# Kernel tuning notes

Hardware: AMD Instinct MI355X
Metric: run time of the kernel (lower is better)

The kernel has to match this reference:

```python
import jax, jax.numpy as jnp
import numpy as np

EPS = 1e-6
SEARCH_RANGE = 4  # K = 2*R+1 = 9


def setup_inputs() -> dict:
    key = jax.random.key(0)
    k1, k2, k3, k4 = jax.random.split(key, 4)
    B, C, H, W = 4, 128, 128, 240
    E = 64
    F_L = jax.random.normal(k1, (B, C, H, W), dtype=jnp.float32)
    F_R = jax.random.normal(k2, (B, C, H, W), dtype=jnp.float32)
    d0 = jax.random.uniform(k3, (B, 1, H, W), dtype=jnp.float32) * 64.0  # pixel disparity
    phi_w = jax.random.normal(k4, (E, C), dtype=jnp.float32) / np.sqrt(C)  # 1x1 conv weight
    return {"F_L": F_L, "F_R": F_R, "d0": d0, "phi_w": phi_w}


def _embed(x, phi_w):
    # 1x1 conv + channel L2 normalize (cosine embedding)
    y = jnp.einsum('ec,bchw->behw', phi_w, x)
    norm = jnp.sqrt(jnp.sum(y * y, axis=1, keepdims=True)) + EPS
    return y / norm


def reference(F_L, F_R, d0, phi_w):
    R = SEARCH_RANGE
    FL = _embed(F_L, phi_w)  # (B,E,H,W)
    FR = _embed(F_R, phi_w)
    B, E, H, W = FL.shape
    deltas = jnp.arange(-R, R + 1, dtype=FL.dtype)  # (K,)
    xx = jnp.arange(W, dtype=FL.dtype)  # base x grid
    # x' = x - (d0 + delta); align_corners=True grid round-trips to pixel coords exactly,
    # y coordinate is identity, so warp is 1D bilinear along W with border clamp.
    xprime = xx[None, None, None, :] - d0[:, None, 0, :, :] - deltas[None, :, None, None]  # (B,K,H,W)
    x0 = jnp.floor(xprime)
    w = xprime - x0  # bilinear weight
    i0 = jnp.clip(x0.astype(jnp.int32), 0, W - 1)
    i1 = jnp.clip(x0.astype(jnp.int32) + 1, 0, W - 1)
    FR_e = FR[:, None]  # (B,1,E,H,W)
    g0 = jnp.take_along_axis(FR_e, i0[:, :, None, :, :], axis=4)  # (B,K,E,H,W)
    g1 = jnp.take_along_axis(FR_e, i1[:, :, None, :, :], axis=4)
    FR_s = g0 * (1.0 - w)[:, :, None] + g1 * w[:, :, None]
    cost_vol = jnp.einsum('behw,bkehw->bkhw', FL, FR_s)  # (B,K,H,W)
    return cost_vol
```

## Files before the change

### kernel.cpp

```cpp
#include <hip/hip_runtime.h>
#include <hip/hip_bf16.h>

#define NB 4
#define NC 128
#define NH 128
#define NW 240
#define NE 64
#define NK 9
#define PLANE (NH*NW)
#define CHW (NC*PLANE)

typedef __attribute__((ext_vector_type(8))) short short8;
typedef __attribute__((ext_vector_type(4))) float f32x4;
typedef __attribute__((ext_vector_type(2))) __fp16 fp16x2;
typedef __attribute__((ext_vector_type(8))) __fp16 fp16x8;

__device__ __forceinline__ unsigned pkh(float x, float y){
  fp16x2 h = __builtin_amdgcn_cvt_pkrtz(x, y);
  return __builtin_bit_cast(unsigned, h);
}
__device__ __forceinline__ float fdot2u(unsigned a, unsigned b, float c){
#if __has_builtin(__builtin_amdgcn_fdot2)
  return __builtin_amdgcn_fdot2(__builtin_bit_cast(fp16x2,a),
                                __builtin_bit_cast(fp16x2,b), c, false);
#else
  fp16x2 ha = __builtin_bit_cast(fp16x2,a), hb = __builtin_bit_cast(fp16x2,b);
  return c + (float)ha[0]*(float)hb[0] + (float)ha[1]*(float)hb[1];
#endif
}
__device__ __forceinline__ int swz(int r){ return (r ^ (r>>3)) & 7; }

__device__ __forceinline__ void gload_lds16(const float* g, float* lds_u, int lane){
#if __has_builtin(__builtin_amdgcn_global_load_lds)
  __builtin_amdgcn_global_load_lds(
      (const __attribute__((address_space(1))) unsigned*)g,
      (__attribute__((address_space(3))) unsigned*)lds_u, 16, 0, 0);
#else
  *(float4*)(lds_u + 4*lane) = *(const float4*)g;
#endif
}

#define WAITB(N) do {                                                        \
    asm volatile("s_waitcnt vmcnt(" #N ") lgkmcnt(0)" ::: "memory");         \
    __builtin_amdgcn_s_barrier();                                            \
    __builtin_amdgcn_sched_barrier(0);                                       \
  } while (0)

__global__ __launch_bounds__(1024, 4)
void fused_kernel(const float* __restrict__ xL,
                  const float* __restrict__ xR,
                  const float* __restrict__ d0g,
                  const float* __restrict__ phig,
                  float* __restrict__ outg)
{
  __shared__ __attribute__((aligned(16))) float bufs[4*7680];
  __shared__ __attribute__((aligned(16))) unsigned short phis[NE*136];

  const int tid  = threadIdx.x;
  const int lane = tid & 63;
  const int wv   = tid >> 6;
  const int b    = blockIdx.x >> 7;
  const int h    = blockIdx.x & 127;
  const size_t base = (size_t)b*CHW + (size_t)h*NW;
  const int pixbase = (b*NH + h)*NW;

  const int mrow = lane & 15;
  const int kg   = lane >> 4;
  const int nt   = wv;
  const int n    = 16*nt + mrow;

  auto issue_chunk = [&](int q){
    const float* src = (q < 4) ? xL : xR;
    const int cb = 32*(q & 3);
    float* buf = &bufs[(q & 3)*7680];
    #pragma unroll
    for (int i = 0; i < 2; ++i) {
      int qq = 2*wv + i;
      if (qq < 30) {
        int g4 = qq*64 + lane;
        int c = g4/60, s4 = g4 - 60*c;
        gload_lds16(src + base + (size_t)(cb + c)*PLANE + 4*s4,
                    buf + qq*256, lane);
      }
    }
  };

  auto gemm_round = [&](const float* bf, int cb, f32x4 (&acc)[4]){
    if (nt < 15) {
      fp16x8 bv;
      #pragma unroll
      for (int j = 0; j < 8; ++j)
        bv[j] = (__fp16)bf[(8*kg + j)*240 + n];
      #pragma unroll
      for (int mt = 0; mt < 4; ++mt) {
        short8 raw = *(const short8*)&phis[(16*mt + mrow)*136 + cb + 8*kg];
        fp16x8 af = __builtin_bit_cast(fp16x8, raw);
        acc[mt] = __builtin_amdgcn_mfma_f32_16x16x32_f16(af, bv, acc[mt], 0, 0, 0);
      }
    }
  };

  auto norm_pack = [&](f32x4 (&acc)[4], uint2 (&pk)[4]){
    float ss = 0.f;
    #pragma unroll
    for (int mt = 0; mt < 4; ++mt)
      #pragma unroll
      for (int r = 0; r < 4; ++r)
        ss += acc[mt][r]*acc[mt][r];
    ss += __shfl_xor(ss, 16, 64);
    ss += __shfl_xor(ss, 32, 64);
    float inv = 1.f/(sqrtf(ss) + 1e-6f);
    #pragma unroll
    for (int mt = 0; mt < 4; ++mt) {
      pk[mt].x = pkh(acc[mt][0]*inv, acc[mt][1]*inv);
      pk[mt].y = pkh(acc[mt][2]*inv, acc[mt][3]*inv);
    }
  };

  auto frag_write = [&](unsigned short* dst, uint2 (&pk)[4]){
    #pragma unroll
    for (int mt = 0; mt < 4; ++mt) {
      int e0 = 16*mt + 4*kg;
      int pos = n*64 + (((e0>>3) ^ swz(n))<<3) + (e0&7);
      *(uint2*)&dst[pos] = pk[mt];
    }
  };

  float d0v = (tid < 960) ? d0g[pixbase + (tid >> 2)] : 0.f;
  float4 pr[2];
  #pragma unroll
  for (int i = 0; i < 2; ++i) {
    int idx = i*1024 + tid;
    pr[i] = *(const float4*)(phig + (idx>>5)*128 + 4*(idx&31));
  }
  issue_chunk(0);
  issue_chunk(1);
  issue_chunk(2);
  #pragma unroll
  for (int i = 0; i < 2; ++i) {
    int idx = i*1024 + tid;
    uint2 pk; pk.x = pkh(pr[i].x, pr[i].y); pk.y = pkh(pr[i].z, pr[i].w);
    *(uint2*)&phis[(idx>>5)*136 + 4*(idx&31)] = pk;
  }

  f32x4 accL[4], accR[4];
  #pragma unroll
  for (int mt = 0; mt < 4; ++mt) {
    accL[mt] = (f32x4){0.f,0.f,0.f,0.f};
    accR[mt] = (f32x4){0.f,0.f,0.f,0.f};
  }
  uint2 flpk[4], frpk[4];

  WAITB(4); issue_chunk(3); gemm_round(&bufs[0*7680],  0, accL);
  WAITB(4); issue_chunk(4); gemm_round(&bufs[1*7680], 32, accL);
  WAITB(4); issue_chunk(5); gemm_round(&bufs[2*7680], 64, accL);
  WAITB(4); issue_chunk(6); gemm_round(&bufs[3*7680], 96, accL);
  if (nt < 15) norm_pack(accL, flpk);
  WAITB(4); issue_chunk(7); gemm_round(&bufs[0*7680],  0, accR);
  WAITB(4);                 gemm_round(&bufs[1*7680], 32, accR);
  WAITB(2);                 gemm_round(&bufs[2*7680], 64, accR);
  WAITB(0);                 gemm_round(&bufs[3*7680], 96, accR);
  if (nt < 15) norm_pack(accR, frpk);

  unsigned short* FLb = (unsigned short*)&bufs[0*7680];
  unsigned short* FRb = (unsigned short*)&bufs[1*7680];
  if (nt < 15) {
    frag_write(FLb, flpk);
    frag_write(FRb, frpk);
  }
  __syncthreads();

  float* cvb = (float*)phis;
  if (tid < 960) {
    const int p  = tid >> 2;
    const int eh = tid & 3;
    float xf  = (float)p - d0v;
    float x0  = floorf(xf);
    float wfr = xf - x0;
    int jb = (int)x0 - 4;

    unsigned fl[8];
    #pragma unroll
    for (int i = 0; i < 2; ++i) {
      int c4 = 2*eh + i;
      uint4 raw = *(const uint4*)&FLb[p*64 + ((c4 ^ swz(p))<<3)];
      fl[4*i+0]=raw.x; fl[4*i+1]=raw.y; fl[4*i+2]=raw.z; fl[4*i+3]=raw.w;
    }

    float D[10];
    #pragma unroll
    for (int t = 0; t < 10; ++t) {
      int j = jb + t;
      j = j < 0 ? 0 : (j > NW-1 ? NW-1 : j);
      float s = 0.f;
      #pragma unroll
      for (int i = 0; i < 2; ++i) {
        int c4 = 2*eh + i;
        uint4 raw = *(const uint4*)&FRb[j*64 + ((c4 ^ swz(j))<<3)];
        s = fdot2u(fl[4*i+0], raw.x, s);
        s = fdot2u(fl[4*i+1], raw.y, s);
        s = fdot2u(fl[4*i+2], raw.z, s);
        s = fdot2u(fl[4*i+3], raw.w, s);
      }
      D[t] = s;
    }
    #pragma unroll
    for (int t = 0; t < 10; ++t) {
      D[t] += __shfl_xor(D[t], 1, 64);
      D[t] += __shfl_xor(D[t], 2, 64);
    }

    #define WK(k) { const int t0 = 8-(k); cvb[(k)*NW + p] = (1.f - wfr)*D[t0] + wfr*D[t0+1]; }
    if      (eh == 0) { WK(0) WK(1) WK(2) }
    else if (eh == 1) { WK(3) WK(4) }
    else if (eh == 2) { WK(5) WK(6) }
    else              { WK(7) WK(8) }
    #undef WK
  }
  __syncthreads();

  if (tid < 540) {
    int k = tid/60, w4 = tid - 60*k;
    float4 v = *(const float4*)&cvb[k*NW + 4*w4];
    *(float4*)(outg + (size_t)b*NK*PLANE + (size_t)h*NW + (size_t)k*PLANE + 4*w4) = v;
  }
}

extern "C" void kernel_launch(void* const* d_in, const int* in_sizes, int n_in,
                              void* d_out, int out_size, void* d_ws, size_t ws_size,
                              hipStream_t stream) {
  const float* xL   = (const float*)d_in[0];
  const float* xR   = (const float*)d_in[1];
  const float* d0g  = (const float*)d_in[2];
  const float* phig = (const float*)d_in[3];
  float* outg = (float*)d_out;
  fused_kernel<<<dim3(NB*NH), dim3(1024), 0, stream>>>(xL, xR, d0g, phig, outg);
}
```

Measured before the change: 153.7 us.

## Process two image rows per block with half-depth channel chunks

Each block now handles two image rows (480 pixels) instead of one, so the grid halves to one block per CU. The channel pipeline becomes 16 chunks of 16 channels, and each wave computes two N-tiles. The aim is to amortise the phi load, pipeline fill and block launch costs over more pixels and to avoid a second partial wave of blocks. In exchange, the K=32 MFMA is fed only 16 real channels, with half its inputs zero-padded, and there are twice as many barrier-synchronised pipeline steps.

```diff
diff --git a/kernel.cpp b/kernel.cpp
--- a/kernel.cpp
+++ b/kernel.cpp
@@ -9,6 +9,7 @@
 #define NK 9
 #define PLANE (NH*NW)
 #define CHW (NC*PLANE)
+#define P2 480
 
 typedef __attribute__((ext_vector_type(8))) short short8;
 typedef __attribute__((ext_vector_type(4))) float f32x4;
@@ -59,112 +60,145 @@
   const int tid  = threadIdx.x;
   const int lane = tid & 63;
   const int wv   = tid >> 6;
-  const int b    = blockIdx.x >> 7;
-  const int h    = blockIdx.x & 127;
-  const size_t base = (size_t)b*CHW + (size_t)h*NW;
-  const int pixbase = (b*NH + h)*NW;
+  const int b    = blockIdx.x >> 6;
+  const int hp   = blockIdx.x & 63;
+  const size_t base = (size_t)b*CHW + (size_t)hp*P2;
+  const int pixbase = b*PLANE + hp*P2;
 
   const int mrow = lane & 15;
   const int kg   = lane >> 4;
-  const int nt   = wv;
-  const int n    = 16*nt + mrow;
 
   auto issue_chunk = [&](int q){
-    const float* src = (q < 4) ? xL : xR;
-    const int cb = 32*(q & 3);
+    const float* src = (q < 8) ? xL : xR;
+    const int kq = q & 7;
     float* buf = &bufs[(q & 3)*7680];
     #pragma unroll
     for (int i = 0; i < 2; ++i) {
       int qq = 2*wv + i;
       if (qq < 30) {
         int g4 = qq*64 + lane;
-        int c = g4/60, s4 = g4 - 60*c;
-        gload_lds16(src + base + (size_t)(cb + c)*PLANE + 4*s4,
+        int c = g4/120, s4 = g4 - 120*c;
+        gload_lds16(src + base + (size_t)(16*kq + c)*PLANE + 4*s4,
                     buf + qq*256, lane);
       }
     }
   };
 
-  auto gemm_round = [&](const float* bf, int cb, f32x4 (&acc)[4]){
-    if (nt < 15) {
-      fp16x8 bv;
-      #pragma unroll
-      for (int j = 0; j < 8; ++j)
-        bv[j] = (__fp16)bf[(8*kg + j)*240 + n];
+  auto gemm_round = [&](int q, f32x4 (&acc)[2][4]){
+    const int kq = q & 7;
+    const float* bf = &bufs[(q & 3)*7680];
+    if (wv < 15) {
+      short8 rawA[4];
+      #pragma unroll
+      for (int mt = 0; mt < 4; ++mt) rawA[mt] = (short8){0,0,0,0,0,0,0,0};
+      if (kg < 2) {
+        #pragma unroll
+        for (int mt = 0; mt < 4; ++mt)
+          rawA[mt] = *(const short8*)&phis[(16*mt + mrow)*136 + 16*kq + 8*kg];
+      }
+      #pragma unroll
+      for (int tt = 0; tt < 2; ++tt) {
+        const int n = 16*(wv + 15*tt) + mrow;
+        fp16x8 bv;
+        #pragma unroll
+        for (int j = 0; j < 8; ++j) bv[j] = (__fp16)0.f;
+        if (kg < 2) {
+          #pragma unroll
+          for (int j = 0; j < 8; ++j)
+            bv[j] = (__fp16)bf[(8*kg + j)*P2 + n];
+        }
+        #pragma unroll
+        for (int mt = 0; mt < 4; ++mt) {
+          fp16x8 af = __builtin_bit_cast(fp16x8, rawA[mt]);
+          acc[tt][mt] = __builtin_amdgcn_mfma_f32_16x16x32_f16(af, bv, acc[tt][mt], 0, 0, 0);
+        }
+      }
+    }
+  };
+
+  auto norm_pack = [&](f32x4 (&acc)[2][4], uint2 (&pk)[2][4]){
+    #pragma unroll
+    for (int tt = 0; tt < 2; ++tt) {
+      float ss = 0.f;
+      #pragma unroll
+      for (int mt = 0; mt < 4; ++mt)
+        #pragma unroll
+        for (int r = 0; r < 4; ++r)
+          ss += acc[tt][mt][r]*acc[tt][mt][r];
+      ss += __shfl_xor(ss, 16, 64);
+      ss += __shfl_xor(ss, 32, 64);
+      float inv = 1.f/(sqrtf(ss) + 1e-6f);
       #pragma unroll
       for (int mt = 0; mt < 4; ++mt) {
-        short8 raw = *(const short8*)&phis[(16*mt + mrow)*136 + cb + 8*kg];
-        fp16x8 af = __builtin_bit_cast(fp16x8, raw);
-        acc[mt] = __builtin_amdgcn_mfma_f32_16x16x32_f16(af, bv, acc[mt], 0, 0, 0);
-      }
-    }
-  };
-
-  auto norm_pack = [&](f32x4 (&acc)[4], uint2 (&pk)[4]){
-    float ss = 0.f;
-    #pragma unroll
-    for (int mt = 0; mt < 4; ++mt)
-      #pragma unroll
-      for (int r = 0; r < 4; ++r)
-        ss += acc[mt][r]*acc[mt][r];
-    ss += __shfl_xor(ss, 16, 64);
-    ss += __shfl_xor(ss, 32, 64);
-    float inv = 1.f/(sqrtf(ss) + 1e-6f);
-    #pragma unroll
-    for (int mt = 0; mt < 4; ++mt) {
-      pk[mt].x = pkh(acc[mt][0]*inv, acc[mt][1]*inv);
-      pk[mt].y = pkh(acc[mt][2]*inv, acc[mt][3]*inv);
-    }
-  };
-
-  auto frag_write = [&](unsigned short* dst, uint2 (&pk)[4]){
-    #pragma unroll
-    for (int mt = 0; mt < 4; ++mt) {
-      int e0 = 16*mt + 4*kg;
-      int pos = n*64 + (((e0>>3) ^ swz(n))<<3) + (e0&7);
-      *(uint2*)&dst[pos] = pk[mt];
-    }
-  };
-
-  float d0v = (tid < 960) ? d0g[pixbase + (tid >> 2)] : 0.f;
+        pk[tt][mt].x = pkh(acc[tt][mt][0]*inv, acc[tt][mt][1]*inv);
+        pk[tt][mt].y = pkh(acc[tt][mt][2]*inv, acc[tt][mt][3]*inv);
+      }
+    }
+  };
+
+  auto frag_write = [&](unsigned short* dst, uint2 (&pk)[2][4]){
+    #pragma unroll
+    for (int tt = 0; tt < 2; ++tt) {
+      const int n = 16*(wv + 15*tt) + mrow;
+      #pragma unroll
+      for (int mt = 0; mt < 4; ++mt) {
+        int e0 = 16*mt + 4*kg;
+        int pos = n*64 + (((e0>>3) ^ swz(n))<<3) + (e0&7);
+        *(uint2*)&dst[pos] = pk[tt][mt];
+      }
+    }
+  };
+
+  float d0v = (tid < 960) ? d0g[pixbase + (tid >> 1)] : 0.f;
   float4 pr[2];
   #pragma unroll
   for (int i = 0; i < 2; ++i) {
     int idx = i*1024 + tid;
     pr[i] = *(const float4*)(phig + (idx>>5)*128 + 4*(idx&31));
   }
-  issue_chunk(0);
-  issue_chunk(1);
-  issue_chunk(2);
   #pragma unroll
   for (int i = 0; i < 2; ++i) {
     int idx = i*1024 + tid;
     uint2 pk; pk.x = pkh(pr[i].x, pr[i].y); pk.y = pkh(pr[i].z, pr[i].w);
     *(uint2*)&phis[(idx>>5)*136 + 4*(idx&31)] = pk;
   }
-
-  f32x4 accL[4], accR[4];
-  #pragma unroll
-  for (int mt = 0; mt < 4; ++mt) {
-    accL[mt] = (f32x4){0.f,0.f,0.f,0.f};
-    accR[mt] = (f32x4){0.f,0.f,0.f,0.f};
-  }
-  uint2 flpk[4], frpk[4];
-
-  WAITB(4); issue_chunk(3); gemm_round(&bufs[0*7680],  0, accL);
-  WAITB(4); issue_chunk(4); gemm_round(&bufs[1*7680], 32, accL);
-  WAITB(4); issue_chunk(5); gemm_round(&bufs[2*7680], 64, accL);
-  WAITB(4); issue_chunk(6); gemm_round(&bufs[3*7680], 96, accL);
-  if (nt < 15) norm_pack(accL, flpk);
-  WAITB(4); issue_chunk(7); gemm_round(&bufs[0*7680],  0, accR);
-  WAITB(4);                 gemm_round(&bufs[1*7680], 32, accR);
-  WAITB(2);                 gemm_round(&bufs[2*7680], 64, accR);
-  WAITB(0);                 gemm_round(&bufs[3*7680], 96, accR);
-  if (nt < 15) norm_pack(accR, frpk);
-
-  unsigned short* FLb = (unsigned short*)&bufs[0*7680];
-  unsigned short* FRb = (unsigned short*)&bufs[1*7680];
-  if (nt < 15) {
+  issue_chunk(0); issue_chunk(1); issue_chunk(2);
+
+  f32x4 accL[2][4], accR[2][4];
+  #pragma unroll
+  for (int tt = 0; tt < 2; ++tt)
+    #pragma unroll
+    for (int mt = 0; mt < 4; ++mt) {
+      accL[tt][mt] = (f32x4){0.f,0.f,0.f,0.f};
+      accR[tt][mt] = (f32x4){0.f,0.f,0.f,0.f};
+    }
+  uint2 flpk[2][4], frpk[2][4];
+
+  WAITB(4); issue_chunk(3);  gemm_round(0,  accL);
+  WAITB(4); issue_chunk(4);  gemm_round(1,  accL);
+  WAITB(4); issue_chunk(5);  gemm_round(2,  accL);
+  WAITB(4); issue_chunk(6);  gemm_round(3,  accL);
+  WAITB(4); issue_chunk(7);  gemm_round(4,  accL);
+  WAITB(4); issue_chunk(8);  gemm_round(5,  accL);
+  WAITB(4); issue_chunk(9);  gemm_round(6,  accL);
+  WAITB(4); issue_chunk(10); gemm_round(7,  accL);
+  if (wv < 15) norm_pack(accL, flpk);
+  WAITB(4); issue_chunk(11); gemm_round(8,  accR);
+  WAITB(4); issue_chunk(12); gemm_round(9,  accR);
+  WAITB(4); issue_chunk(13); gemm_round(10, accR);
+  WAITB(4); issue_chunk(14); gemm_round(11, accR);
+  WAITB(4); issue_chunk(15); gemm_round(12, accR);
+  WAITB(4);                  gemm_round(13, accR);
+  WAITB(2);                  gemm_round(14, accR);
+  WAITB(0);                  gemm_round(15, accR);
+  if (wv < 15) norm_pack(accR, frpk);
+
+  asm volatile("s_waitcnt lgkmcnt(0)" ::: "memory");
+  __builtin_amdgcn_s_barrier();
+  __builtin_amdgcn_sched_barrier(0);
+  unsigned short* FLb = (unsigned short*)&bufs[0];
+  unsigned short* FRb = (unsigned short*)&bufs[2*7680];
+  if (wv < 15) {
     frag_write(FLb, flpk);
     frag_write(FRb, frpk);
   }
@@ -172,17 +206,19 @@
 
   float* cvb = (float*)phis;
   if (tid < 960) {
-    const int p  = tid >> 2;
-    const int eh = tid & 3;
-    float xf  = (float)p - d0v;
+    const int p  = tid >> 1;
+    const int eh = tid & 1;
+    const int row = (p >= NW) ? 1 : 0;
+    const int w   = p - row*NW;
+    float xf  = (float)w - d0v;
     float x0  = floorf(xf);
     float wfr = xf - x0;
-    int jb = (int)x0 - 4;
-
-    unsigned fl[8];
-    #pragma unroll
-    for (int i = 0; i < 2; ++i) {
-      int c4 = 2*eh + i;
+    int jbl = (int)x0 - 4;
+
+    unsigned fl[16];
+    #pragma unroll
+    for (int i = 0; i < 4; ++i) {
+      int c4 = 4*eh + i;
       uint4 raw = *(const uint4*)&FLb[p*64 + ((c4 ^ swz(p))<<3)];
       fl[4*i+0]=raw.x; fl[4*i+1]=raw.y; fl[4*i+2]=raw.z; fl[4*i+3]=raw.w;
     }
@@ -190,12 +226,13 @@
     float D[10];
     #pragma unroll
     for (int t = 0; t < 10; ++t) {
-      int j = jb + t;
+      int j = jbl + t;
       j = j < 0 ? 0 : (j > NW-1 ? NW-1 : j);
+      j += row*NW;
       float s = 0.f;
       #pragma unroll
-      for (int i = 0; i < 2; ++i) {
-        int c4 = 2*eh + i;
+      for (int i = 0; i < 4; ++i) {
+        int c4 = 4*eh + i;
         uint4 raw = *(const uint4*)&FRb[j*64 + ((c4 ^ swz(j))<<3)];
         s = fdot2u(fl[4*i+0], raw.x, s);
         s = fdot2u(fl[4*i+1], raw.y, s);
@@ -205,24 +242,32 @@
       D[t] = s;
     }
     #pragma unroll
-    for (int t = 0; t < 10; ++t) {
-      D[t] += __shfl_xor(D[t], 1, 64);
-      D[t] += __shfl_xor(D[t], 2, 64);
-    }
-
-    #define WK(k) { const int t0 = 8-(k); cvb[(k)*NW + p] = (1.f - wfr)*D[t0] + wfr*D[t0+1]; }
-    if      (eh == 0) { WK(0) WK(1) WK(2) }
-    else if (eh == 1) { WK(3) WK(4) }
-    else if (eh == 2) { WK(5) WK(6) }
-    else              { WK(7) WK(8) }
-    #undef WK
+    for (int t = 0; t < 10; ++t) D[t] += __shfl_xor(D[t], 1, 64);
+
+    if (eh == 0) {
+      #pragma unroll
+      for (int k = 0; k < 5; ++k) {
+        int t0 = 8 - k;
+        cvb[k*P2 + p] = (1.f - wfr)*D[t0] + wfr*D[t0+1];
+      }
+    } else {
+      #pragma unroll
+      for (int k = 5; k < 9; ++k) {
+        int t0 = 8 - k;
+        cvb[k*P2 + p] = (1.f - wfr)*D[t0] + wfr*D[t0+1];
+      }
+    }
   }
   __syncthreads();
 
-  if (tid < 540) {
-    int k = tid/60, w4 = tid - 60*k;
-    float4 v = *(const float4*)&cvb[k*NW + 4*w4];
-    *(float4*)(outg + (size_t)b*NK*PLANE + (size_t)h*NW + (size_t)k*PLANE + 4*w4) = v;
+  #pragma unroll
+  for (int i = 0; i < 2; ++i) {
+    int t = i*1024 + tid;
+    if (t < 1080) {
+      int k = t/120, w4 = t - 120*k;
+      float4 v = *(const float4*)&cvb[k*P2 + 4*w4];
+      *(float4*)(outg + (size_t)(b*NK + k)*PLANE + (size_t)hp*P2 + 4*w4) = v;
+    }
   }
 }
 
@@ -234,5 +279,5 @@
   const float* d0g  = (const float*)d_in[2];
   const float* phig = (const float*)d_in[3];
   float* outg = (float*)d_out;
-  fused_kernel<<<dim3(NB*NH), dim3(1024), 0, stream>>>(xL, xR, d0g, phig, outg);
-}
+  fused_kernel<<<dim3(NB*NH/2), dim3(1024), 0, stream>>>(xL, xR, d0g, phig, outg);
+}
```

New measurement: 152.7 us. No clear change (-0.6%).
